# Optimization experiments

Measured on AMD Instinct MI355X. Metric: run time of the kernel, lower is better.

## Reference

```python
import jax, jax.numpy as jnp
import numpy as np

EPS = 1e-10
MARGIN = 0.05
DELTA = 0.1
H = W = 512
N = 8388608


def setup_inputs() -> dict:
    key = jax.random.key(0)
    k1, k2, k3, k4 = jax.random.split(key, 4)
    v_input = jax.random.uniform(k1, (3, H, W), dtype=jnp.float32)
    coords = jax.random.randint(k2, (N, 4), 0, W, dtype=jnp.int32)  # x1,y1,x2,y2
    darker = jax.random.randint(k3, (N,), 0, 3, dtype=jnp.int32)
    weights = jax.random.uniform(k4, (N,), dtype=jnp.float32)
    return {"v_input": v_input, "coords": coords, "darker": darker, "weights": weights}


def reference(v_input, coords, darker, weights):
    # v = sum over channels / 3, then affine remap (exactly as torch code)
    v = jnp.sum(v_input, axis=0) / 3.0
    v = (v * 255.0 + 1.0) / 256.0  # [H, W]

    x1, y1, x2, y2 = coords[:, 0], coords[:, 1], coords[:, 2], coords[:, 3]
    r1 = v[y1, x1]
    r2 = v[y2, x2]
    ratio = r1 / (r2 + EPS)
    ratio_inv = r2 / (r1 + EPS)

    b = 1.0 + DELTA + MARGIN
    inv_b = 1.0 / b
    # darker == 1: penalize if ratio > 1/b
    l1 = jnp.where(ratio > inv_b, (ratio - inv_b) + (b - ratio_inv), 0.0)
    # darker == 2: penalize if ratio < b
    l2 = jnp.where(ratio < b, (b - ratio) + (ratio_inv - inv_b), 0.0)
    # darker == 0 (margin <= delta branch): two-sided hinge around [bl, br]
    br = 1.0 + DELTA - MARGIN
    bl = 1.0 / br
    l0 = jnp.where(
        ratio > br,
        (ratio - br) + (bl - ratio_inv),
        jnp.where(ratio < bl, (bl - ratio) + (ratio_inv - br), 0.0),
    )

    per = jnp.where(darker == 1, l1, jnp.where(darker == 2, l2, l0))
    loss = jnp.sum(weights * per) / np.float32(coords.shape[0])
    return loss
```

## Files before the change

### kernel.cpp

```cpp
#include <hip/hip_runtime.h>

#define HW 512
#define NPIX (HW * HW)
#define LDS_PIX 81920
#define THREADS 1024
#define BLOCKS 512
#define NB 2
#define RNDS 8

#define EPS_F  1e-10f
constexpr double B_d  = 1.0 + 0.1 + 0.05;
constexpr double BR_d = 1.0 + 0.1 - 0.05;
#define B_F    ((float)B_d)
#define INVB_F ((float)(1.0 / B_d))
#define BR_F   ((float)BR_d)
#define BL_F   ((float)(1.0 / BR_d))

typedef __attribute__((ext_vector_type(4))) int ivec4;

__global__ void build_v(const float* __restrict__ vin,
                        unsigned char* __restrict__ vq,
                        float* __restrict__ out) {
    int i = blockIdx.x * blockDim.x + threadIdx.x;
    if (i == 0) *out = 0.0f;
    if (i < NPIX) {
        float s = vin[i] + vin[i + NPIX] + vin[i + 2 * NPIX];
        float m = s * (1.0f / 3.0f);
        vq[i] = (unsigned char)__float2int_rn(m * 255.0f);
    }
}

__device__ __forceinline__ float rcp_fast(float x) {
#if __has_builtin(__builtin_amdgcn_rcpf)
    return __builtin_amdgcn_rcpf(x);
#else
    return 1.0f / x;
#endif
}

__device__ __forceinline__ float per_loss(float r1, float r2, int d) {
    float ratio = r1 * rcp_fast(r2 + EPS_F);
    float rinv  = r2 * rcp_fast(r1 + EPS_F);
    float l1 = (ratio > INVB_F) ? (ratio - INVB_F + (B_F - rinv)) : 0.0f;
    float l2 = (ratio < B_F)    ? (B_F - ratio + (rinv - INVB_F)) : 0.0f;
    float l0 = (ratio > BR_F)   ? (ratio - BR_F + (BL_F - rinv))
             : ((ratio < BL_F)  ? (BL_F - ratio + (rinv - BR_F)) : 0.0f);
    return (d == 1) ? l1 : ((d == 2) ? l2 : l0);
}


__device__ __forceinline__ void load_c(ivec4 (&cc)[NB], const ivec4* __restrict__ coords,
                                       int tid, int T, int ofs) {
    #pragma unroll
    for (int k = 0; k < NB; ++k)
        cc[k] = __builtin_nontemporal_load(&coords[tid + (ofs + k) * T]);
}

__device__ __forceinline__ void load_dw(int (&dd)[NB], float (&ww)[NB],
                                        const int* __restrict__ darker,
                                        const float* __restrict__ weights,
                                        int tid, int T, int ofs) {
    #pragma unroll
    for (int k = 0; k < NB; ++k)
        dd[k] = __builtin_nontemporal_load(&darker[tid + (ofs + k) * T]);
    #pragma unroll
    for (int k = 0; k < NB; ++k)
        ww[k] = __builtin_nontemporal_load(&weights[tid + (ofs + k) * T]);
}

__device__ __forceinline__ void gather_issue(const ivec4 (&cc)[NB],
        unsigned (&q1)[NB], unsigned (&q2)[NB],
        const unsigned char* lv, const unsigned char* __restrict__ vq) {
    #pragma unroll
    for (int k = 0; k < NB; ++k) {
        int i1 = cc[k].y * HW + cc[k].x;
        int i2 = cc[k].w * HW + cc[k].z;
        if (i1 < LDS_PIX) q1[k] = lv[i1]; else q1[k] = vq[i1];
        if (i2 < LDS_PIX) q2[k] = lv[i2]; else q2[k] = vq[i2];
    }
}

__device__ __forceinline__ void consume(const unsigned (&q1)[NB], const unsigned (&q2)[NB],
                                        const int (&dd)[NB], const float (&ww)[NB],
                                        float& acc) {
    #pragma unroll
    for (int k = 0; k < NB; ++k) {
        float r1 = (float)(q1[k] + 1) * (1.0f / 256.0f);
        float r2 = (float)(q2[k] + 1) * (1.0f / 256.0f);
        acc += ww[k] * per_loss(r1, r2, dd[k]);
    }
}

#define SBAR() __builtin_amdgcn_sched_barrier(0)

__global__ __launch_bounds__(THREADS)
void whdr_kernel(
        const unsigned char* __restrict__ vq,
        const ivec4* __restrict__ coords,
        const int*   __restrict__ darker,
        const float* __restrict__ weights,
        float*       __restrict__ out,
        int n) {
    __shared__ unsigned char lv[LDS_PIX];
    const int tid = blockIdx.x * THREADS + threadIdx.x;
    const int T   = BLOCKS * THREADS;
    float acc = 0.0f;

    if (n == T * NB * RNDS) {
        ivec4 cA[NB], cB[NB];
        int   dA[NB], dB[NB];
        float wA[NB], wB[NB];
        unsigned qA1[NB], qA2[NB], qB1[NB], qB2[NB];

        load_c (cA, coords, tid, T, 0);
        load_dw(dA, wA, darker, weights, tid, T, 0);
        load_c (cB, coords, tid, T, NB);
        load_dw(dB, wB, darker, weights, tid, T, NB);
        {
            const uint4* s4 = (const uint4*)vq;
            uint4* d4 = (uint4*)lv;
            #pragma unroll
            for (int j = threadIdx.x; j < LDS_PIX / 16; j += THREADS) d4[j] = s4[j];
        }
        __syncthreads();
        gather_issue(cA, qA1, qA2, lv, vq);            SBAR();

#define RPF(r, CUR, NXT) \
        gather_issue(c##NXT, q##NXT##1, q##NXT##2, lv, vq);        SBAR(); \
        load_c (c##CUR, coords, tid, T, (r + 2) * NB);             SBAR(); \
        consume(q##CUR##1, q##CUR##2, d##CUR, w##CUR, acc); \
        load_dw(d##CUR, w##CUR, darker, weights, tid, T, (r + 2) * NB); SBAR();

        RPF(0, A, B)
        RPF(1, B, A)
        RPF(2, A, B)
        RPF(3, B, A)
        RPF(4, A, B)
        RPF(5, B, A)
#undef RPF
        gather_issue(cB, qB1, qB2, lv, vq);            SBAR();
        consume(qA1, qA2, dA, wA, acc);
        consume(qB1, qB2, dB, wB, acc);
    } else {
        {
            const uint4* s4 = (const uint4*)vq;
            uint4* d4 = (uint4*)lv;
            for (int j = threadIdx.x; j < LDS_PIX / 16; j += THREADS) d4[j] = s4[j];
        }
        __syncthreads();
        const int TT = gridDim.x * THREADS;
        for (int i = tid; i < n; i += TT) {
            ivec4 c = coords[i];
            int i1 = c.y * HW + c.x, i2 = c.w * HW + c.z;
            unsigned a = (i1 < LDS_PIX) ? (unsigned)lv[i1] : (unsigned)vq[i1];
            unsigned b = (i2 < LDS_PIX) ? (unsigned)lv[i2] : (unsigned)vq[i2];
            float r1 = (float)(a + 1) * (1.0f / 256.0f);
            float r2 = (float)(b + 1) * (1.0f / 256.0f);
            acc += weights[i] * per_loss(r1, r2, darker[i]);
        }
    }

    #pragma unroll
    for (int off = 32; off > 0; off >>= 1)
        acc += __shfl_down(acc, off, 64);
    __syncthreads();
    float* wsum = (float*)lv;
    int lane = threadIdx.x & 63;
    int wid  = threadIdx.x >> 6;
    if (lane == 0) wsum[wid] = acc;
    __syncthreads();
    if (threadIdx.x == 0) {
        float s = 0.0f;
        #pragma unroll
        for (int i = 0; i < THREADS / 64; ++i) s += wsum[i];
        atomicAdd(out, s / (float)n);
    }
}

extern "C" void kernel_launch(void* const* d_in, const int* in_sizes, int n_in,
                              void* d_out, int out_size, void* d_ws, size_t ws_size,
                              hipStream_t stream) {
    const float* v_input = (const float*)d_in[0];
    const ivec4* coords  = (const ivec4*)d_in[1];
    const int*   darker  = (const int*)d_in[2];
    const float* weights = (const float*)d_in[3];
    float* out = (float*)d_out;
    unsigned char* vq = (unsigned char*)d_ws;
    int n = in_sizes[2];

    build_v<<<(NPIX + 255) / 256, 256, 0, stream>>>(v_input, vq, out);
    whdr_kernel<<<BLOCKS, THREADS, 0, stream>>>(vq, coords, darker, weights, out, n);
}
```

Measured before the change: 263.4 us.

## Double LDS image cache and pair per-thread elements for vector loads

Raises the LDS-resident portion of the quantized image from 80K to 160K pixels so more gathers hit shared memory instead of global memory. It also changes the work mapping so each thread handles two adjacent elements per step, letting darker and weights be fetched as 8-byte vector loads and coordinates as contiguous pairs. The larger LDS footprint reduces blocks resident per CU and lengthens the per-block fill copy, and the wider per-thread stride may change coalescing.

```diff
diff --git a/kernel.cpp b/kernel.cpp
--- a/kernel.cpp
+++ b/kernel.cpp
@@ -2,10 +2,9 @@
 
 #define HW 512
 #define NPIX (HW * HW)
-#define LDS_PIX 81920
+#define LDS_PIX 163840
 #define THREADS 1024
 #define BLOCKS 512
-#define NB 2
 #define RNDS 8
 
 #define EPS_F  1e-10f
@@ -16,7 +15,9 @@
 #define BR_F   ((float)BR_d)
 #define BL_F   ((float)(1.0 / BR_d))
 
-typedef __attribute__((ext_vector_type(4))) int ivec4;
+typedef __attribute__((ext_vector_type(4))) int   ivec4;
+typedef __attribute__((ext_vector_type(2))) int   ivec2;
+typedef __attribute__((ext_vector_type(2))) float fvec2;
 
 __global__ void build_v(const float* __restrict__ vin,
                         unsigned char* __restrict__ vq,
@@ -49,30 +50,25 @@
 }
 
 
-__device__ __forceinline__ void load_c(ivec4 (&cc)[NB], const ivec4* __restrict__ coords,
-                                       int tid, int T, int ofs) {
-    #pragma unroll
-    for (int k = 0; k < NB; ++k)
-        cc[k] = __builtin_nontemporal_load(&coords[tid + (ofs + k) * T]);
+__device__ __forceinline__ void load_c(ivec4 (&cc)[2], const ivec4* __restrict__ coords,
+                                       int pp) {
+    cc[0] = __builtin_nontemporal_load(&coords[2 * pp]);
+    cc[1] = __builtin_nontemporal_load(&coords[2 * pp + 1]);
 }
 
-__device__ __forceinline__ void load_dw(int (&dd)[NB], float (&ww)[NB],
+__device__ __forceinline__ void load_dw(ivec2& dd, fvec2& ww,
                                         const int* __restrict__ darker,
                                         const float* __restrict__ weights,
-                                        int tid, int T, int ofs) {
-    #pragma unroll
-    for (int k = 0; k < NB; ++k)
-        dd[k] = __builtin_nontemporal_load(&darker[tid + (ofs + k) * T]);
-    #pragma unroll
-    for (int k = 0; k < NB; ++k)
-        ww[k] = __builtin_nontemporal_load(&weights[tid + (ofs + k) * T]);
+                                        int pp) {
+    dd = __builtin_nontemporal_load((const ivec2*)&darker[2 * pp]);
+    ww = __builtin_nontemporal_load((const fvec2*)&weights[2 * pp]);
 }
 
-__device__ __forceinline__ void gather_issue(const ivec4 (&cc)[NB],
-        unsigned (&q1)[NB], unsigned (&q2)[NB],
+__device__ __forceinline__ void gather_issue(const ivec4 (&cc)[2],
+        unsigned (&q1)[2], unsigned (&q2)[2],
         const unsigned char* lv, const unsigned char* __restrict__ vq) {
     #pragma unroll
-    for (int k = 0; k < NB; ++k) {
+    for (int k = 0; k < 2; ++k) {
         int i1 = cc[k].y * HW + cc[k].x;
         int i2 = cc[k].w * HW + cc[k].z;
         if (i1 < LDS_PIX) q1[k] = lv[i1]; else q1[k] = vq[i1];
@@ -80,11 +76,11 @@
     }
 }
 
-__device__ __forceinline__ void consume(const unsigned (&q1)[NB], const unsigned (&q2)[NB],
-                                        const int (&dd)[NB], const float (&ww)[NB],
+__device__ __forceinline__ void consume(const unsigned (&q1)[2], const unsigned (&q2)[2],
+                                        const ivec2& dd, const fvec2& ww,
                                         float& acc) {
     #pragma unroll
-    for (int k = 0; k < NB; ++k) {
+    for (int k = 0; k < 2; ++k) {
         float r1 = (float)(q1[k] + 1) * (1.0f / 256.0f);
         float r2 = (float)(q2[k] + 1) * (1.0f / 256.0f);
         acc += ww[k] * per_loss(r1, r2, dd[k]);
@@ -106,16 +102,16 @@
     const int T   = BLOCKS * THREADS;
     float acc = 0.0f;
 
-    if (n == T * NB * RNDS) {
-        ivec4 cA[NB], cB[NB];
-        int   dA[NB], dB[NB];
-        float wA[NB], wB[NB];
-        unsigned qA1[NB], qA2[NB], qB1[NB], qB2[NB];
+    if (n == T * 2 * RNDS) {
+        ivec4 cA[2], cB[2];
+        ivec2 dA, dB;
+        fvec2 wA, wB;
+        unsigned qA1[2], qA2[2], qB1[2], qB2[2];
 
-        load_c (cA, coords, tid, T, 0);
-        load_dw(dA, wA, darker, weights, tid, T, 0);
-        load_c (cB, coords, tid, T, NB);
-        load_dw(dB, wB, darker, weights, tid, T, NB);
+        load_c (cA, coords, tid + 0 * T);
+        load_dw(dA, wA, darker, weights, tid + 0 * T);
+        load_c (cB, coords, tid + 1 * T);
+        load_dw(dB, wB, darker, weights, tid + 1 * T);
         {
             const uint4* s4 = (const uint4*)vq;
             uint4* d4 = (uint4*)lv;
@@ -127,9 +123,9 @@
 
 #define RPF(r, CUR, NXT) \
         gather_issue(c##NXT, q##NXT##1, q##NXT##2, lv, vq);        SBAR(); \
-        load_c (c##CUR, coords, tid, T, (r + 2) * NB);             SBAR(); \
+        load_c (c##CUR, coords, tid + (r + 2) * T);                SBAR(); \
         consume(q##CUR##1, q##CUR##2, d##CUR, w##CUR, acc); \
-        load_dw(d##CUR, w##CUR, darker, weights, tid, T, (r + 2) * NB); SBAR();
+        load_dw(d##CUR, w##CUR, darker, weights, tid + (r + 2) * T); SBAR();
 
         RPF(0, A, B)
         RPF(1, B, A)
```

New measurement: 251.7 us. 1.05x faster.
